# Performance work log

Measured on AMD Instinct MI355X. Metric: run time of the kernel, lower is better.

## Reference

```python
import jax, jax.numpy as jnp
import numpy as np

_R, _C = 64, 64
_N = _R * _C
_SEC_PER_A = 31556926.0
_K = 0.01        # sheet_conductivity
_ALPHA = 1.25    # sheet_flow_exp
_HR = 0.1        # bedrock_step_height
_LR = 2.0        # cavity_spacing
_A = 5e-25       # cavity_closure_coeff
_NEXP = 3        # Glen exponent


def _build_grid():
    idx = np.arange(_N).reshape(_R, _C)
    tail = np.concatenate([idx[:, :-1].ravel(), idx[:-1, :].ravel()]).astype(np.int32)
    head = np.concatenate([idx[:, 1:].ravel(), idx[1:, :].ravel()]).astype(np.int32)
    L = tail.size
    links_at_node = -np.ones((_N, 4), np.int32)
    adj = -np.ones((_N, 4), np.int32)
    cnt = np.zeros(_N, np.int32)
    for l in range(L):
        for a, b in ((tail[l], head[l]), (head[l], tail[l])):
            links_at_node[a, cnt[a]] = l
            adj[a, cnt[a]] = b
            cnt[a] += 1
    r, c = np.divmod(np.arange(_N), _C)
    status = ((r == 0) | (r == _R - 1) | (c == 0) | (c == _C - 1)).astype(np.int32)
    return tail, head, links_at_node, adj, status


def setup_inputs():
    key = jax.random.key(0)
    k = jax.random.split(key, 8)
    tail, head, links_at_node, adj, status = _build_grid()
    L = tail.size
    bedrock = jax.random.uniform(k[0], (_N,), jnp.float32, 0.0, 500.0)
    ice_thk = jax.random.uniform(k[1], (_N,), jnp.float32, 100.0, 1000.0)
    overburden = 917.0 * 9.81 * ice_thk
    base_potential = 1000.0 * 9.81 * bedrock + overburden
    potential = base_potential - 0.3 * overburden + 1e3 * jax.random.normal(k[2], (_N,), jnp.float32)
    sheet_thickness = jax.random.uniform(k[3], (_N,), jnp.float32, 0.01, 0.1)
    sliding_velocity = jax.random.uniform(k[4], (L,), jnp.float32, 10.0, 100.0)
    specific_melt_rate = jax.random.uniform(k[5], (_N,), jnp.float32, 1e-7, 1e-6)
    link_length = jnp.full((L,), 100.0, jnp.float32)
    adj_j = jnp.asarray(adj)
    # mean over ALL 4 slots, padded entries contribute 0 (matches original jnp.mean)
    adj_pot = jnp.mean(jnp.where(adj_j != -1, base_potential[adj_j], 0.0), axis=1)
    inflow = jnp.where(base_potential > adj_pot, 1, -1) * (jnp.asarray(status) > 0)
    return dict(
        base_potential=base_potential,
        overburden_pressure=overburden,
        specific_melt_rate=specific_melt_rate,
        sheet_thickness=sheet_thickness,
        potential=potential,
        sliding_velocity=sliding_velocity,
        link_length=link_length,
        link_tail=jnp.asarray(tail),
        link_head=jnp.asarray(head),
        links_at_node=jnp.asarray(links_at_node),
        inflow_outflow=inflow.astype(jnp.int32),
        dt=3600,
    )


def reference(base_potential, overburden_pressure, specific_melt_rate, sheet_thickness,
              potential, sliding_velocity, link_length, link_tail, link_head,
              links_at_node, inflow_outflow, dt):
    N = base_potential.shape[0]
    t, h = link_tail, link_head
    # --- elliptic operator assembly (per-link, scatter into dense [N,N]) ---
    sheets = 0.5 * (sheet_thickness[t] + sheet_thickness[h])
    inv_grad = jnp.abs((potential[t] - potential[h]) / link_length) ** (-0.5)
    c = -_K * sheets ** _ALPHA * link_length * inv_grad  # symmetric link coefficient (<0)
    dir_row = inflow_outflow == 1  # Dirichlet rows
    ct = jnp.where(dir_row[t], 0.0, c)  # contribution into row tail
    ch = jnp.where(dir_row[h], 0.0, c)  # contribution into row head
    M = (jnp.zeros((N, N), base_potential.dtype)
         .at[t, h].add(ct).at[h, t].add(ch)
         .at[t, t].add(-ct).at[h, h].add(-ch))
    M = jnp.where(dir_row[:, None], jnp.eye(N, dtype=M.dtype), M)
    forcing = jnp.where(dir_row, base_potential - overburden_pressure, specific_melt_rate)
    new_potential = jnp.linalg.solve(M, forcing)
    # --- sheet thickness: map_mean_of_links_to_node then Newton on node-local ODE ---
    valid = links_at_node != -1
    lv = (sliding_velocity / _SEC_PER_A)[links_at_node]  # [N,4]
    sliding = jnp.abs(jnp.sum(jnp.where(valid, lv, 0.0), axis=1)
                      / jnp.maximum(valid.sum(axis=1), 1))
    pressure = base_potential - new_potential
    dtf = jnp.asarray(dt, base_potential.dtype)
    # residual r(h) = h - h0 - dt*(sliding*(HR-h)/LR - A*P^n*h) is LINEAR in h,
    # so Newton converges in one exact step -> closed form:
    new_h = (sheet_thickness + dtf * sliding * _HR / _LR) / (
        1.0 + dtf * (sliding / _LR + _A * pressure ** _NEXP))
    return new_potential, new_h
```

## Files before the change

kernel.cpp:

```cpp
#include <hip/hip_runtime.h>
#include <math.h>


#define NT    512
#define NPT   8
#define NN    4096
#define NC    1024
#define NCC   256
#define CCIT  20
#define MAXIT 40

enum : int { RSHL1 = 0x101, RSHR1 = 0x111,
             ROR8 = 0x128, ROR12 = 0x12C, ROR14 = 0x12E, ROR15 = 0x12F,
             WSHL1 = 0x130, WSHR1 = 0x138 };

__device__ __forceinline__ void barL() {
    asm volatile("s_waitcnt lgkmcnt(0)" ::: "memory");
    __builtin_amdgcn_s_barrier();
    asm volatile("" ::: "memory");
}

template<int CTRL>
__device__ __forceinline__ float dppf(float x) {
    return __int_as_float(__builtin_amdgcn_update_dpp(
        __float_as_int(x), __float_as_int(x), CTRL, 0xF, 0xF, false));
}
template<int CTRL>
__device__ __forceinline__ double dppd(double x) {
    const int lo = __double2loint(x), hi = __double2hiint(x);
    const int l2 = __builtin_amdgcn_update_dpp(lo, lo, CTRL, 0xF, 0xF, false);
    const int h2 = __builtin_amdgcn_update_dpp(hi, hi, CTRL, 0xF, 0xF, false);
    return __hiloint2double(h2, l2);
}
__device__ __forceinline__ void pl16sw(int& a, int& b) {
    asm volatile("s_nop 1\n\tv_permlane16_swap_b32 %0, %1" : "+v"(a), "+v"(b));
}
__device__ __forceinline__ void pl32sw(int& a, int& b) {
    asm volatile("s_nop 1\n\tv_permlane32_swap_b32 %0, %1" : "+v"(a), "+v"(b));
}
__device__ __forceinline__ float shift_dn16(float x, bool inR2) {
    int a = __float_as_int(x), b = __float_as_int(x);
    pl16sw(a, b);
    int g = b, g2 = b;
    pl32sw(g, g2);
    return __int_as_float(inR2 ? g : a);
}
__device__ __forceinline__ float shift_up16(float x, bool inR1) {
    int a = __float_as_int(x), b = __float_as_int(x);
    pl16sw(a, b);
    int d1 = __float_as_int(x), d2 = __float_as_int(x);
    pl32sw(d1, d2);
    int e1 = d2, e2 = d2;
    pl16sw(e1, e2);
    return __int_as_float(inR1 ? e1 : b);
}
__device__ __forceinline__ double dsw32(double x) {
    int lo = __double2loint(x), hi = __double2hiint(x);
    int a = lo, b = lo; pl32sw(a, b);
    int c = hi, d = hi; pl32sw(c, d);
    return __hiloint2double(d, b);
}
__device__ __forceinline__ double dsw16(double x) {
    int lo = __double2loint(x), hi = __double2hiint(x);
    int a = lo, b = lo; pl16sw(a, b);
    int c = hi, d = hi; pl16sw(c, d);
    return __hiloint2double(d, b);
}

__global__ __launch_bounds__(NT, 1)
void sds_solver(const float* __restrict__ base_pot,
                const float* __restrict__ ovb,
                const float* __restrict__ melt,
                const float* __restrict__ sheet,
                const float* __restrict__ pot,
                const float* __restrict__ svel,
                const float* __restrict__ llen,
                const int*   __restrict__ ltail,
                const int*   __restrict__ lhead,
                const int*   __restrict__ lan,
                const int*   __restrict__ inflow,
                const int*   __restrict__ dt_raw,
                float* __restrict__ out,
                int N, int L)
{
    __shared__ __align__(16) float cW[NN], cE[NN], cN[NN], cS[NN];
    __shared__ __align__(16) float FD[NN];
    __shared__ __align__(16) float BNDA[8*128], BNDB[8*128];
    __shared__ __align__(16) float CB[32 + NC + 32];
    __shared__ __align__(16) float CB2[32 + NC + 32];
    __shared__ __align__(16) float EB[32 + NC + 32];
    __shared__ __align__(16) float IDC[32 + NC + 32];
    __shared__ __align__(16) float ccb[NCC];
    __shared__ __align__(16) float cWc_s[NC], cEc_s[NC], cNc_s[NC], cSc_s[NC], dc_s[NC];
    __shared__ double redp[32], redg[16];

    const int tid  = threadIdx.x;
    const int lane = tid & 63;
    const int wid  = tid >> 6;
    const int nb0  = (wid << 9) + lane;

    if (N != NN || L != 8064) return;

    const int dti = dt_raw[0];
    const float as_f = __int_as_float(dti);
    const double dtf = (as_f > 0.5f && as_f < 1.0e12f) ? (double)as_f : (double)dti;

    const float invthf = 0.8f;
    const float c1f = 0.2195122f, c2f = 0.9756098f;
    const float wA = 1.75f;

    {
        const float4 z4 = make_float4(0.f, 0.f, 0.f, 0.f);
        #pragma unroll
        for (int i = tid; i < NN/4; i += NT) {
            ((float4*)cW)[i] = z4; ((float4*)cE)[i] = z4;
            ((float4*)cN)[i] = z4; ((float4*)cS)[i] = z4;
        }
        if (tid < 32) {
            CB[tid]=0.f;  CB[32+NC+tid]=0.f;
            CB2[tid]=0.f; CB2[32+NC+tid]=0.f;
            EB[tid]=0.f;  EB[32+NC+tid]=0.f;
            IDC[tid]=0.f; IDC[32+NC+tid]=0.f;
        }
    }
    __syncthreads();

    for (int l = tid; l < 8064; l += NT) {
        int t, h;
        if (l < 4032) {
            const int r = l / 63;
            const int c2 = l - r * 63;
            t = (r << 6) + c2; h = t + 1;
        } else {
            t = l - 4032; h = t + 64;
        }
        const float sheets = 0.5f * (sheet[t] + sheet[h]);
        const float len = llen[l];
        const float grad = fabsf((pot[t] - pot[h]) / len);
        const float c = -0.01f * (sheets * sqrtf(sqrtf(sheets))) * len / sqrtf(grad);
        const bool dt_ = (inflow[t] == 1);
        const bool dh_ = (inflow[h] == 1);
        if (l < 4032) { cE[t] = dt_ ? 0.f : c; cW[h] = dh_ ? 0.f : c; }
        else          { cS[t] = dt_ ? 0.f : c; cN[h] = dh_ ? 0.f : c; }
    }
    __syncthreads();

    float cw[NPT], ce[NPT], cn[NPT], cs[NPT], dgf[NPT], invdf[NPT];
    double bb[NPT], gg[NPT], xv[NPT], rv[NPT];
    bool dirf[NPT];
    auto ldco = [&]() {
        #pragma unroll
        for (int k = 0; k < NPT; ++k) {
            const int n = nb0 + (k << 6);
            cw[k] = cW[n]; ce[k] = cE[n]; cn[k] = cN[n]; cs[k] = cS[n];
        }
    };
    ldco();
    double gsum = 0.0, gcnt = 0.0;
    #pragma unroll
    for (int k = 0; k < NPT; ++k) {
        const int n = nb0 + (k << 6);
        const bool dir = (inflow[n] == 1);
        const double g = (double)base_pot[n] - (double)ovb[n];
        const double d = -((double)cw[k] + (double)ce[k] + (double)cn[k] + (double)cs[k]);
        const double dg = (dir || d == 0.0) ? 1.0 : d;
        dgf[k] = (float)dg; invdf[k] = (float)(1.0 / dg);
        bb[k] = dir ? g : (double)melt[n];
        gg[k] = g; dirf[k] = dir;
        if (dir) { gsum += g; gcnt += 1.0; }
    }
    {
        #pragma unroll
        for (int off = 32; off > 0; off >>= 1) {
            gsum += __shfl_down(gsum, off, 64);
            gcnt += __shfl_down(gcnt, off, 64);
        }
        if (lane == 0) { redg[2*wid] = gsum; redg[2*wid+1] = gcnt; }
        __syncthreads();
        gsum = 0.0; gcnt = 0.0;
        #pragma unroll
        for (int w = 0; w < NT/64; ++w) { gsum += redg[2*w]; gcnt += redg[2*w+1]; }
    }
    const double gmean = gsum / (gcnt > 0.0 ? gcnt : 1.0);

    auto stB = [&](float* B, const float* v) {
        *(float2*)&B[(wid << 7) + (lane << 1)] = make_float2(v[0], v[7]);
    };
    float qf[NPT];
    auto spmvC = [&](const float* B, const float* vr) {
        const float nb = B[(((wid + 7) & 7) << 7) + (lane << 1) + 1];
        const float sb = B[(((wid + 1) & 7) << 7) + (lane << 1) + 0];
        #pragma unroll
        for (int k = 0; k < NPT; ++k) {
            const float wv = dppf<WSHR1>(vr[k]);
            const float ev = dppf<WSHL1>(vr[k]);
            const float nv = k ? vr[k-1] : nb;
            const float sv = (k < NPT-1) ? vr[k+1] : sb;
            qf[k] = dgf[k]*vr[k] + cw[k]*wv + ce[k]*ev + cn[k]*nv + cs[k]*sv;
        }
    };

    {
        float x0r[NPT];
        #pragma unroll
        for (int k = 0; k < NPT; ++k) {
            const float x0f = (float)(dirf[k] ? gg[k] : gmean);
            xv[k] = (double)x0f; x0r[k] = x0f;
        }
        stB(BNDA, x0r); __syncthreads();
        spmvC(BNDA, x0r);
        #pragma unroll
        for (int k = 0; k < NPT; ++k)
            rv[k] = dirf[k] ? 0.0 : (bb[k] - (double)qf[k]);
    }
    __syncthreads();

    {
        #pragma unroll
        for (int k = 0; k < NPT; ++k) {
            const int n = nb0 + (k << 6);
            if (lane != 0  && inflow[n-1]  == 1) cW[n] = 0.f;
            if (lane != 63 && inflow[n+1]  == 1) cE[n] = 0.f;
            if (n >= 64        && inflow[n-64] == 1) cN[n] = 0.f;
            if (n < NN-64      && inflow[n+64] == 1) cS[n] = 0.f;
            FD[n] = dirf[k] ? 0.f : dgf[k];
        }
    }
    __syncthreads();
    ldco();

    #pragma unroll
    for (int q = 0; q < 2; ++q) {
        const int I = 2*tid + q;
        const int R = tid >> 4, C = I & 31;
        const int na = 128*R + 2*C, nbq = na+1, nc_ = na+64, nd = na+65;
        cEc_s[I] = cE[nbq] + cE[nd];
        cWc_s[I] = cW[na] + cW[nc_];
        cNc_s[I] = cN[na] + cN[nbq];
        cSc_s[I] = cS[nc_] + cS[nd];
        const float d = FD[na]+FD[nbq]+FD[nc_]+FD[nd]
                      + 2.0f*(cE[na] + cE[nc_] + cS[na] + cS[nbq]);
        dc_s[I] = (d > 0.f) ? d : 1.0f;
    }
    __syncthreads();

    float cwc[2], cec[2], cnc[2], csc[2], dcr[2], invdc[2];
    {
        float2 t;
        t = *(float2*)&cWc_s[2*tid]; cwc[0]=t.x; cwc[1]=t.y;
        t = *(float2*)&cEc_s[2*tid]; cec[0]=t.x; cec[1]=t.y;
        t = *(float2*)&cNc_s[2*tid]; cnc[0]=t.x; cnc[1]=t.y;
        t = *(float2*)&cSc_s[2*tid]; csc[0]=t.x; csc[1]=t.y;
        t = *(float2*)&dc_s[2*tid];  dcr[0]=t.x; dcr[1]=t.y;
        invdc[0] = 1.0f/dcr[0]; invdc[1] = 1.0f/dcr[1];
        *(float2*)&IDC[32 + 2*tid] = make_float2(invdc[0], invdc[1]);
    }
    float cwcc[4], cecc[4], cncc[4], cscc[4], dccr[4], invdcc[4];
    if (tid < 64) {
        #pragma unroll
        for (int j = 0; j < 4; ++j) {
            const int Rc = ((tid >> 4) << 2) + j, Cc = tid & 15;
            const int IA = 64*Rc + 2*Cc, IB = IA+1, IC = IA+32, ID = IA+33;
            cecc[j] = cEc_s[IB] + cEc_s[ID];
            cwcc[j] = cWc_s[IA] + cWc_s[IC];
            cncc[j] = cNc_s[IA] + cNc_s[IB];
            cscc[j] = cSc_s[IC] + cSc_s[ID];
            const float d = dc_s[IA]+dc_s[IB]+dc_s[IC]+dc_s[ID]
                          + 2.0f*(cEc_s[IA] + cEc_s[IC] + cSc_s[IA] + cSc_s[IB]);
            dccr[j] = (d > 0.f) ? d : 1.0f;
            invdcc[j] = 1.0f/dccr[j];
        }
    }
    float c1cc[CCIT+1], c2cc[CCIT+1], invthcc;
    {
        const double a = 8e-3, b2 = 2.0;
        const double th = 0.5*(b2+a), de = 0.5*(b2-a), s1 = th/de;
        double rp = 1.0/s1;
        for (int j = 1; j <= CCIT; ++j) {
            const double rj = 1.0/(2.0*s1 - rp);
            c1cc[j] = (float)(rj*rp);
            c2cc[j] = (float)(2.0*rj/de);
            rp = rj;
        }
        invthcc = (float)(1.0/th);
    }
    auto cspmv = [&](const float* B_, float v0, float v1, float& q0, float& q1) {
        const float2 up = *(const float2*)&B_[2*tid];
        const float2 dn = *(const float2*)&B_[64 + 2*tid];
        const float wv = dppf<WSHR1>(v1);
        const float ev = dppf<WSHL1>(v0);
        q0 = dcr[0]*v0 + cwc[0]*wv + cec[0]*v1 + cnc[0]*up.x + csc[0]*dn.x;
        q1 = dcr[1]*v1 + cwc[1]*v0 + cec[1]*ev + cnc[1]*up.y + csc[1]*dn.y;
    };

    double rho_prev = 0.0, pap = 0.0, tol = 0.0;
    double pv[NPT], sv[NPT], rpv[NPT];
    #pragma unroll
    for (int k = 0; k < NPT; ++k) { pv[k]=0.0; sv[k]=0.0; rpv[k]=0.0; }

    for (int it = 0; it < MAXIT; ++it) {
        float f0[NPT], d0[NPT], d1[NPT], zpre[NPT];
        #pragma unroll
        for (int k = 0; k < NPT; ++k) { f0[k] = (float)rv[k] * invdf[k]; d0[k] = f0[k] * invthf; }
        stB(BNDA, d0); barL();
        spmvC(BNDA, d0);
        #pragma unroll
        for (int k = 0; k < NPT; ++k) {
            const float f1 = f0[k] - qf[k]*invdf[k];
            d1[k] = c1f*d0[k] + c2f*f1;
            zpre[k] = d0[k] + d1[k];
            f0[k] = f1;
        }
        stB(BNDB, d1); barL();
        spmvC(BNDB, d1);

        float r1[NPT], t2[NPT];
        #pragma unroll
        for (int k = 0; k < NPT; ++k) {
            const float fres = f0[k] - qf[k]*invdf[k];
            r1[k] = dirf[k] ? 0.f : dgf[k]*fres;
        }
        #pragma unroll
        for (int k = 0; k < NPT; ++k) t2[k] = r1[k] + dppf<WSHL1>(r1[k]);
        if ((lane & 1) == 0) {
            #pragma unroll
            for (int j = 0; j < 4; ++j)
                CB2[32 + ((wid << 2) + j)*32 + (lane >> 1)] = t2[2*j] + t2[2*j+1];
        }
        barL();

        float rc[2], f0c[2], d0c[2], d1c[2], qc0, qc1;
        {
            const float2 rcl = *(const float2*)&CB2[32 + 2*tid];
            rc[0] = rcl.x; rc[1] = rcl.y;
        }
        #pragma unroll
        for (int q = 0; q < 2; ++q) {
            f0c[q] = rc[q] * invdc[q];
            d0c[q] = f0c[q] * invthf;
        }
        {
            const float2 ru = *(const float2*)&CB2[2*tid];
            const float2 rd = *(const float2*)&CB2[64 + 2*tid];
            const float2 iu = *(const float2*)&IDC[2*tid];
            const float2 id = *(const float2*)&IDC[64 + 2*tid];
            const float wv = dppf<WSHR1>(d0c[1]);
            const float ev = dppf<WSHL1>(d0c[0]);
            qc0 = dcr[0]*d0c[0] + cwc[0]*wv + cec[0]*d0c[1]
                + cnc[0]*((ru.x*iu.x)*invthf) + csc[0]*((rd.x*id.x)*invthf);
            qc1 = dcr[1]*d0c[1] + cwc[1]*d0c[0] + cec[1]*ev
                + cnc[1]*((ru.y*iu.y)*invthf) + csc[1]*((rd.y*id.y)*invthf);
        }
        {
            const float f1a = f0c[0] - qc0*invdc[0];
            const float f1b = f0c[1] - qc1*invdc[1];
            d1c[0] = c1f*d0c[0] + c2f*f1a;
            d1c[1] = c1f*d0c[1] + c2f*f1b;
            f0c[0] = f1a; f0c[1] = f1b;
        }
        *(float2*)&EB[32 + 2*tid] = make_float2(d1c[0], d1c[1]);
        barL();
        cspmv(EB, d1c[0], d1c[1], qc0, qc1);
        {
            const float fra = f0c[0] - qc0*invdc[0];
            const float frb = f0c[1] - qc1*invdc[1];
            *(float2*)&CB[32 + 2*tid] = make_float2(dcr[0]*fra, dcr[1]*frb);
        }
        barL();

        if (tid < 64) {
            const int cc_c  = tid & 15;
            const int cc_rb = tid >> 4;
            const bool inR1 = (cc_rb == 1), inR2 = (cc_rb == 2);
            float fr[4], dr[4], zc[4];
            #pragma unroll
            for (int j = 0; j < 4; ++j) {
                const int IA = (((cc_rb << 2) + j) << 6) + (cc_c << 1);
                const float rcc = CB[32+IA] + CB[32+IA+1] + CB[32+IA+32] + CB[32+IA+33];
                fr[j] = rcc * invdcc[j];
                dr[j] = fr[j] * invthcc;
                zc[j] = dr[j];
            }
            for (int s = 1; s <= CCIT; ++s) {
                const float zN = shift_dn16(dr[3], inR2);
                const float zS = shift_up16(dr[0], inR1);
                float qcc[4];
                #pragma unroll
                for (int j = 0; j < 4; ++j) {
                    const float wj = dppf<RSHR1>(dr[j]);
                    const float ej = dppf<RSHL1>(dr[j]);
                    const float nj = j ? dr[j-1] : zN;
                    const float sj = (j < 3) ? dr[j+1] : zS;
                    qcc[j] = dccr[j]*dr[j] + cwcc[j]*wj + cecc[j]*ej
                           + cncc[j]*nj + cscc[j]*sj;
                }
                #pragma unroll
                for (int j = 0; j < 4; ++j) {
                    fr[j] -= qcc[j] * invdcc[j];
                    dr[j]  = c1cc[s]*dr[j] + c2cc[s]*fr[j];
                    zc[j] += dr[j];
                }
            }
            #pragma unroll
            for (int j = 0; j < 4; ++j)
                ccb[(((cc_rb << 2) + j) << 4) + cc_c] = zc[j];
        }
        barL();

        const float ecv = wA * ccb[16*(tid >> 5) + (tid & 15)];
        float zmc[2] = { d0c[0] + d1c[0] + ecv, d0c[1] + d1c[1] + ecv };
        {
            const float2 ru = *(const float2*)&CB2[2*tid];
            const float2 rd = *(const float2*)&CB2[64 + 2*tid];
            const float2 iu = *(const float2*)&IDC[2*tid];
            const float2 id = *(const float2*)&IDC[64 + 2*tid];
            const float2 du = *(const float2*)&EB[2*tid];
            const float2 dd = *(const float2*)&EB[64 + 2*tid];
            const int R = tid >> 4;
            const int Ru = (R > 0)  ? R - 1 : 0;
            const int Rd = (R < 31) ? R + 1 : 31;
            const float ecu = wA * ccb[(Ru >> 1)*16 + (tid & 15)];
            const float ecd = wA * ccb[(Rd >> 1)*16 + (tid & 15)];
            const float upx = ((ru.x*iu.x)*invthf + du.x) + ecu;
            const float upy = ((ru.y*iu.y)*invthf + du.y) + ecu;
            const float dnx = ((rd.x*id.x)*invthf + dd.x) + ecd;
            const float dny = ((rd.y*id.y)*invthf + dd.y) + ecd;
            const float wv = dppf<WSHR1>(zmc[1]);
            const float ev = dppf<WSHL1>(zmc[0]);
            qc0 = dcr[0]*zmc[0] + cwc[0]*wv + cec[0]*zmc[1] + cnc[0]*upx + csc[0]*dnx;
            qc1 = dcr[1]*zmc[1] + cwc[1]*zmc[0] + cec[1]*ev + cnc[1]*upy + csc[1]*dny;
        }
        float fmc[2] = { (rc[0]-qc0)*invdc[0], (rc[1]-qc1)*invdc[1] };
        float d0p[2] = { fmc[0]*invthf, fmc[1]*invthf };
        *(float2*)&CB[32 + 2*tid] = make_float2(d0p[0], d0p[1]);
        barL();
        cspmv(CB, d0p[0], d0p[1], qc0, qc1);
        {
            const float f1a = fmc[0] - qc0*invdc[0];
            const float f1b = fmc[1] - qc1*invdc[1];
            const float efa = zmc[0] + c1f*d0p[0] + c2f*f1a + d0p[0];
            const float efb = zmc[1] + c1f*d0p[1] + c2f*f1b + d0p[1];
            *(float2*)&EB[32 + 2*tid] = make_float2(efa, efb);
        }
        barL();

        float ec[4];
        #pragma unroll
        for (int j = 0; j < 4; ++j)
            ec[j] = EB[32 + ((wid << 2) + j)*32 + (lane >> 1)];
        float zmid[NPT], zf[NPT];
        #pragma unroll
        for (int k = 0; k < NPT; ++k)
            zmid[k] = zpre[k] + (dirf[k] ? 0.f : wA * ec[k >> 1]);
        stB(BNDA, zmid); barL();
        spmvC(BNDA, zmid);
        float fmid[NPT], d0q[NPT];
        #pragma unroll
        for (int k = 0; k < NPT; ++k) {
            fmid[k] = (float)rv[k]*invdf[k] - qf[k]*invdf[k];
            d0q[k]  = fmid[k] * invthf;
        }
        stB(BNDB, d0q); barL();
        spmvC(BNDB, d0q);
        #pragma unroll
        for (int k = 0; k < NPT; ++k) {
            const float f1 = fmid[k] - qf[k]*invdf[k];
            zf[k] = zmid[k] + d0q[k] + c1f*d0q[k] + c2f*f1;
        }
        stB(BNDA, zf); barL();
        spmvC(BNDA, zf);

        double rho_n = 0.0, rzp = 0.0, zw = 0.0, pw = 0.0;
        #pragma unroll
        for (int k = 0; k < NPT; ++k) {
            const double zk = (double)zf[k], wk = (double)qf[k];
            rho_n += rv[k]  * zk;
            rzp   += rpv[k] * zk;
            zw    += zk * wk;
            pw    += pv[k] * wk;
        }
        rho_n += dsw32(rho_n); rzp += dsw32(rzp); zw += dsw32(zw); pw += dsw32(pw);
        rho_n += dsw16(rho_n); rzp += dsw16(rzp); zw += dsw16(zw); pw += dsw16(pw);
        rho_n += dppd<ROR8 >(rho_n); rzp += dppd<ROR8 >(rzp); zw += dppd<ROR8 >(zw); pw += dppd<ROR8 >(pw);
        rho_n += dppd<ROR12>(rho_n); rzp += dppd<ROR12>(rzp); zw += dppd<ROR12>(zw); pw += dppd<ROR12>(pw);
        rho_n += dppd<ROR14>(rho_n); rzp += dppd<ROR14>(rzp); zw += dppd<ROR14>(zw); pw += dppd<ROR14>(pw);
        rho_n += dppd<ROR15>(rho_n); rzp += dppd<ROR15>(rzp); zw += dppd<ROR15>(zw); pw += dppd<ROR15>(pw);
        if (lane == 0) {
            redp[4*wid] = rho_n; redp[4*wid+1] = rzp;
            redp[4*wid+2] = zw;  redp[4*wid+3] = pw;
        }
        barL();
        rho_n = 0.0; rzp = 0.0; zw = 0.0; pw = 0.0;
        #pragma unroll
        for (int w = 0; w < NT/64; ++w) {
            rho_n += redp[4*w];   rzp += redp[4*w+1];
            zw    += redp[4*w+2]; pw  += redp[4*w+3];
        }

        if (it == 0) {
            tol = rho_n * 1e-3 + 1e-300;
            if (!(rho_n > 0.0)) break;
        } else if (rho_n <= tol || !(rho_n > 0.0)) break;
        const double beta = (it == 0) ? 0.0
                          : fmax(0.0, (rho_n - rzp) / rho_prev);
        pap = zw + beta * (2.0 * pw + beta * pap);
        if (!(pap > 0.0)) break;
        const double alpha = rho_n / pap;
        rho_prev = rho_n;
        #pragma unroll
        for (int k = 0; k < NPT; ++k) {
            rpv[k] = rv[k];
            pv[k] = (double)zf[k] + beta * pv[k];
            sv[k] = (double)qf[k] + beta * sv[k];
            xv[k] += alpha * pv[k];
            rv[k] -= alpha * sv[k];
        }
    }

    #pragma unroll
    for (int k = 0; k < NPT; ++k) {
        const int n = nb0 + (k << 6);
        const int r = (wid << 3) + k, c2 = lane;
        const double x = dirf[k] ? gg[k] : xv[k];

        const int hb = r * 63 + c2;
        float sva = 0.0f; int cnt = 0;
        if (c2 > 0)  { sva += svel[hb - 1];       cnt++; }
        if (c2 < 63) { sva += svel[hb];           cnt++; }
        if (r  > 0)  { sva += svel[4032 + n - 64]; cnt++; }
        if (r  < 63) { sva += svel[4032 + n];      cnt++; }
        const double sliding =
            fabs((double)sva / 31556926.0 / (double)(cnt > 0 ? cnt : 1));
        const double P   = (double)base_pot[n] - x;
        const double num = (double)sheet[n] + dtf * sliding * 0.1 / 2.0;
        const double den = 1.0 + dtf * (sliding / 2.0 + 5e-25 * P * P * P);
        out[n]      = (float)x;
        out[NN + n] = (float)(num / den);
    }
}

extern "C" void kernel_launch(void* const* d_in, const int* in_sizes, int n_in,
                              void* d_out, int out_size, void* d_ws, size_t ws_size,
                              hipStream_t stream) {
    const float* base_pot = (const float*)d_in[0];
    const float* ovb      = (const float*)d_in[1];
    const float* melt     = (const float*)d_in[2];
    const float* sheet    = (const float*)d_in[3];
    const float* pot      = (const float*)d_in[4];
    const float* svel     = (const float*)d_in[5];
    const float* llen     = (const float*)d_in[6];
    const int*   ltail    = (const int*)d_in[7];
    const int*   lhead    = (const int*)d_in[8];
    const int*   lan      = (const int*)d_in[9];
    const int*   inflow   = (const int*)d_in[10];
    const int*   dt_raw   = (const int*)d_in[11];
    float* out = (float*)d_out;
    const int N = in_sizes[0];
    const int L = in_sizes[5];

    hipLaunchKernelGGL(sds_solver, dim3(1), dim3(NT), 0, stream,
                       base_pot, ovb, melt, sheet, pot, svel, llen,
                       ltail, lhead, lan, inflow, dt_raw, out, N, L);
}
```

Baseline: 133.6 us.

## Double block to 1024 threads with four rows per thread

Raises the single workgroup from 512 to 1024 threads (16 waves), so each thread owns 4 grid rows instead of 8. The coarse-grid step now maps one coarse cell per thread instead of two, so the per-thread loops and float2 accesses become scalar ones. The goal is to shorten the serial per-thread work in every PCG iteration of this single-block solver. In exchange, each block-wide reduction now combines 16 wave partials instead of 8, barriers span more waves, and the per-thread register budget is halved at 1024 threads.

Measured after the change: 178.8 us. 33.8% more time.

```diff
diff --git a/kernel.cpp b/kernel.cpp
--- a/kernel.cpp
+++ b/kernel.cpp
@@ -2,8 +2,9 @@
 #include <math.h>
 
 
-#define NT    512
-#define NPT   8
+#define NT    1024
+#define NPT   4
+#define NW    16
 #define NN    4096
 #define NC    1024
 #define NCC   256
@@ -85,19 +86,19 @@
 {
     __shared__ __align__(16) float cW[NN], cE[NN], cN[NN], cS[NN];
     __shared__ __align__(16) float FD[NN];
-    __shared__ __align__(16) float BNDA[8*128], BNDB[8*128];
+    __shared__ __align__(16) float BNDA[NW*128], BNDB[NW*128];
     __shared__ __align__(16) float CB[32 + NC + 32];
     __shared__ __align__(16) float CB2[32 + NC + 32];
     __shared__ __align__(16) float EB[32 + NC + 32];
     __shared__ __align__(16) float IDC[32 + NC + 32];
     __shared__ __align__(16) float ccb[NCC];
     __shared__ __align__(16) float cWc_s[NC], cEc_s[NC], cNc_s[NC], cSc_s[NC], dc_s[NC];
-    __shared__ double redp[32], redg[16];
+    __shared__ double redp[4*NW], redg[2*NW];
 
     const int tid  = threadIdx.x;
     const int lane = tid & 63;
     const int wid  = tid >> 6;
-    const int nb0  = (wid << 9) + lane;
+    const int nb0  = (wid << 8) + lane;
 
     if (N != NN || L != 8064) return;
 
@@ -179,17 +180,17 @@
         __syncthreads();
         gsum = 0.0; gcnt = 0.0;
         #pragma unroll
-        for (int w = 0; w < NT/64; ++w) { gsum += redg[2*w]; gcnt += redg[2*w+1]; }
+        for (int w = 0; w < NW; ++w) { gsum += redg[2*w]; gcnt += redg[2*w+1]; }
     }
     const double gmean = gsum / (gcnt > 0.0 ? gcnt : 1.0);
 
     auto stB = [&](float* B, const float* v) {
-        *(float2*)&B[(wid << 7) + (lane << 1)] = make_float2(v[0], v[7]);
+        *(float2*)&B[(wid << 7) + (lane << 1)] = make_float2(v[0], v[NPT-1]);
     };
     float qf[NPT];
     auto spmvC = [&](const float* B, const float* vr) {
-        const float nb = B[(((wid + 7) & 7) << 7) + (lane << 1) + 1];
-        const float sb = B[(((wid + 1) & 7) << 7) + (lane << 1) + 0];
+        const float nb = B[(((wid + NW-1) & (NW-1)) << 7) + (lane << 1) + 1];
+        const float sb = B[(((wid + 1) & (NW-1)) << 7) + (lane << 1) + 0];
         #pragma unroll
         for (int k = 0; k < NPT; ++k) {
             const float wv = dppf<WSHR1>(vr[k]);
@@ -229,31 +230,25 @@
     __syncthreads();
     ldco();
 
-    #pragma unroll
-    for (int q = 0; q < 2; ++q) {
-        const int I = 2*tid + q;
-        const int R = tid >> 4, C = I & 31;
+    {
+        const int R = tid >> 5, C = tid & 31;
         const int na = 128*R + 2*C, nbq = na+1, nc_ = na+64, nd = na+65;
-        cEc_s[I] = cE[nbq] + cE[nd];
-        cWc_s[I] = cW[na] + cW[nc_];
-        cNc_s[I] = cN[na] + cN[nbq];
-        cSc_s[I] = cS[nc_] + cS[nd];
+        cEc_s[tid] = cE[nbq] + cE[nd];
+        cWc_s[tid] = cW[na] + cW[nc_];
+        cNc_s[tid] = cN[na] + cN[nbq];
+        cSc_s[tid] = cS[nc_] + cS[nd];
         const float d = FD[na]+FD[nbq]+FD[nc_]+FD[nd]
                       + 2.0f*(cE[na] + cE[nc_] + cS[na] + cS[nbq]);
-        dc_s[I] = (d > 0.f) ? d : 1.0f;
+        dc_s[tid] = (d > 0.f) ? d : 1.0f;
     }
     __syncthreads();
 
-    float cwc[2], cec[2], cnc[2], csc[2], dcr[2], invdc[2];
-    {
-        float2 t;
-        t = *(float2*)&cWc_s[2*tid]; cwc[0]=t.x; cwc[1]=t.y;
-        t = *(float2*)&cEc_s[2*tid]; cec[0]=t.x; cec[1]=t.y;
-        t = *(float2*)&cNc_s[2*tid]; cnc[0]=t.x; cnc[1]=t.y;
-        t = *(float2*)&cSc_s[2*tid]; csc[0]=t.x; csc[1]=t.y;
-        t = *(float2*)&dc_s[2*tid];  dcr[0]=t.x; dcr[1]=t.y;
-        invdc[0] = 1.0f/dcr[0]; invdc[1] = 1.0f/dcr[1];
-        *(float2*)&IDC[32 + 2*tid] = make_float2(invdc[0], invdc[1]);
+    float cwc, cec, cnc, csc, dcr, invdc;
+    {
+        cwc = cWc_s[tid]; cec = cEc_s[tid];
+        cnc = cNc_s[tid]; csc = cSc_s[tid];
+        dcr = dc_s[tid];  invdc = 1.0f/dcr;
+        IDC[32 + tid] = invdc;
     }
     float cwcc[4], cecc[4], cncc[4], cscc[4], dccr[4], invdcc[4];
     if (tid < 64) {
@@ -284,13 +279,12 @@
         }
         invthcc = (float)(1.0/th);
     }
-    auto cspmv = [&](const float* B_, float v0, float v1, float& q0, float& q1) {
-        const float2 up = *(const float2*)&B_[2*tid];
-        const float2 dn = *(const float2*)&B_[64 + 2*tid];
-        const float wv = dppf<WSHR1>(v1);
-        const float ev = dppf<WSHL1>(v0);
-        q0 = dcr[0]*v0 + cwc[0]*wv + cec[0]*v1 + cnc[0]*up.x + csc[0]*dn.x;
-        q1 = dcr[1]*v1 + cwc[1]*v0 + cec[1]*ev + cnc[1]*up.y + csc[1]*dn.y;
+    auto cspmv = [&](const float* B_, float v, float& q) {
+        const float up = B_[tid];
+        const float dn = B_[64 + tid];
+        const float wv = dppf<WSHR1>(v);
+        const float ev = dppf<WSHL1>(v);
+        q = dcr*v + cwc*wv + cec*ev + cnc*up + csc*dn;
     };
 
     double rho_prev = 0.0, pap = 0.0, tol = 0.0;
@@ -324,47 +318,34 @@
         for (int k = 0; k < NPT; ++k) t2[k] = r1[k] + dppf<WSHL1>(r1[k]);
         if ((lane & 1) == 0) {
             #pragma unroll
-            for (int j = 0; j < 4; ++j)
-                CB2[32 + ((wid << 2) + j)*32 + (lane >> 1)] = t2[2*j] + t2[2*j+1];
-        }
-        barL();
-
-        float rc[2], f0c[2], d0c[2], d1c[2], qc0, qc1;
+            for (int j = 0; j < 2; ++j)
+                CB2[32 + ((wid << 1) + j)*32 + (lane >> 1)] = t2[2*j] + t2[2*j+1];
+        }
+        barL();
+
+        float rc, f0c, d0c, d1c, qc;
+        rc = CB2[32 + tid];
+        f0c = rc * invdc;
+        d0c = f0c * invthf;
         {
-            const float2 rcl = *(const float2*)&CB2[32 + 2*tid];
-            rc[0] = rcl.x; rc[1] = rcl.y;
-        }
-        #pragma unroll
-        for (int q = 0; q < 2; ++q) {
-            f0c[q] = rc[q] * invdc[q];
-            d0c[q] = f0c[q] * invthf;
+            const float ru = CB2[tid],      rd = CB2[64 + tid];
+            const float iu = IDC[tid],      id = IDC[64 + tid];
+            const float wv = dppf<WSHR1>(d0c);
+            const float ev = dppf<WSHL1>(d0c);
+            qc = dcr*d0c + cwc*wv + cec*ev
+               + cnc*((ru*iu)*invthf) + csc*((rd*id)*invthf);
         }
         {
-            const float2 ru = *(const float2*)&CB2[2*tid];
-            const float2 rd = *(const float2*)&CB2[64 + 2*tid];
-            const float2 iu = *(const float2*)&IDC[2*tid];
-            const float2 id = *(const float2*)&IDC[64 + 2*tid];
-            const float wv = dppf<WSHR1>(d0c[1]);
-            const float ev = dppf<WSHL1>(d0c[0]);
-            qc0 = dcr[0]*d0c[0] + cwc[0]*wv + cec[0]*d0c[1]
-                + cnc[0]*((ru.x*iu.x)*invthf) + csc[0]*((rd.x*id.x)*invthf);
-            qc1 = dcr[1]*d0c[1] + cwc[1]*d0c[0] + cec[1]*ev
-                + cnc[1]*((ru.y*iu.y)*invthf) + csc[1]*((rd.y*id.y)*invthf);
-        }
+            const float f1 = f0c - qc*invdc;
+            d1c = c1f*d0c + c2f*f1;
+            f0c = f1;
+        }
+        EB[32 + tid] = d1c;
+        barL();
+        cspmv(EB, d1c, qc);
         {
-            const float f1a = f0c[0] - qc0*invdc[0];
-            const float f1b = f0c[1] - qc1*invdc[1];
-            d1c[0] = c1f*d0c[0] + c2f*f1a;
-            d1c[1] = c1f*d0c[1] + c2f*f1b;
-            f0c[0] = f1a; f0c[1] = f1b;
-        }
-        *(float2*)&EB[32 + 2*tid] = make_float2(d1c[0], d1c[1]);
-        barL();
-        cspmv(EB, d1c[0], d1c[1], qc0, qc1);
-        {
-            const float fra = f0c[0] - qc0*invdc[0];
-            const float frb = f0c[1] - qc1*invdc[1];
-            *(float2*)&CB[32 + 2*tid] = make_float2(dcr[0]*fra, dcr[1]*frb);
+            const float fra = f0c - qc*invdc;
+            CB[32 + tid] = dcr*fra;
         }
         barL();
 
@@ -407,47 +388,38 @@
         }
         barL();
 
-        const float ecv = wA * ccb[16*(tid >> 5) + (tid & 15)];
-        float zmc[2] = { d0c[0] + d1c[0] + ecv, d0c[1] + d1c[1] + ecv };
+        const int Rq = tid >> 5, Cq = tid & 31;
+        const float ecv = wA * ccb[(Rq >> 1)*16 + (Cq >> 1)];
+        float zmc = d0c + d1c + ecv;
         {
-            const float2 ru = *(const float2*)&CB2[2*tid];
-            const float2 rd = *(const float2*)&CB2[64 + 2*tid];
-            const float2 iu = *(const float2*)&IDC[2*tid];
-            const float2 id = *(const float2*)&IDC[64 + 2*tid];
-            const float2 du = *(const float2*)&EB[2*tid];
-            const float2 dd = *(const float2*)&EB[64 + 2*tid];
-            const int R = tid >> 4;
-            const int Ru = (R > 0)  ? R - 1 : 0;
-            const int Rd = (R < 31) ? R + 1 : 31;
-            const float ecu = wA * ccb[(Ru >> 1)*16 + (tid & 15)];
-            const float ecd = wA * ccb[(Rd >> 1)*16 + (tid & 15)];
-            const float upx = ((ru.x*iu.x)*invthf + du.x) + ecu;
-            const float upy = ((ru.y*iu.y)*invthf + du.y) + ecu;
-            const float dnx = ((rd.x*id.x)*invthf + dd.x) + ecd;
-            const float dny = ((rd.y*id.y)*invthf + dd.y) + ecd;
-            const float wv = dppf<WSHR1>(zmc[1]);
-            const float ev = dppf<WSHL1>(zmc[0]);
-            qc0 = dcr[0]*zmc[0] + cwc[0]*wv + cec[0]*zmc[1] + cnc[0]*upx + csc[0]*dnx;
-            qc1 = dcr[1]*zmc[1] + cwc[1]*zmc[0] + cec[1]*ev + cnc[1]*upy + csc[1]*dny;
-        }
-        float fmc[2] = { (rc[0]-qc0)*invdc[0], (rc[1]-qc1)*invdc[1] };
-        float d0p[2] = { fmc[0]*invthf, fmc[1]*invthf };
-        *(float2*)&CB[32 + 2*tid] = make_float2(d0p[0], d0p[1]);
-        barL();
-        cspmv(CB, d0p[0], d0p[1], qc0, qc1);
+            const float ru = CB2[tid],      rd = CB2[64 + tid];
+            const float iu = IDC[tid],      id = IDC[64 + tid];
+            const float du = EB[tid],       dd = EB[64 + tid];
+            const int Ru = (Rq > 0)  ? Rq - 1 : 0;
+            const int Rd = (Rq < 31) ? Rq + 1 : 31;
+            const float ecu = wA * ccb[(Ru >> 1)*16 + (Cq >> 1)];
+            const float ecd = wA * ccb[(Rd >> 1)*16 + (Cq >> 1)];
+            const float upv = ((ru*iu)*invthf + du) + ecu;
+            const float dnv = ((rd*id)*invthf + dd) + ecd;
+            const float wv = dppf<WSHR1>(zmc);
+            const float ev = dppf<WSHL1>(zmc);
+            qc = dcr*zmc + cwc*wv + cec*ev + cnc*upv + csc*dnv;
+        }
+        float fmc = (rc - qc)*invdc;
+        float d0p = fmc*invthf;
+        CB[32 + tid] = d0p;
+        barL();
+        cspmv(CB, d0p, qc);
         {
-            const float f1a = fmc[0] - qc0*invdc[0];
-            const float f1b = fmc[1] - qc1*invdc[1];
-            const float efa = zmc[0] + c1f*d0p[0] + c2f*f1a + d0p[0];
-            const float efb = zmc[1] + c1f*d0p[1] + c2f*f1b + d0p[1];
-            *(float2*)&EB[32 + 2*tid] = make_float2(efa, efb);
-        }
-        barL();
-
-        float ec[4];
-        #pragma unroll
-        for (int j = 0; j < 4; ++j)
-            ec[j] = EB[32 + ((wid << 2) + j)*32 + (lane >> 1)];
+            const float f1 = fmc - qc*invdc;
+            EB[32 + tid] = zmc + c1f*d0p + c2f*f1 + d0p;
+        }
+        barL();
+
+        float ec[2];
+        #pragma unroll
+        for (int j = 0; j < 2; ++j)
+            ec[j] = EB[32 + ((wid << 1) + j)*32 + (lane >> 1)];
         float zmid[NPT], zf[NPT];
         #pragma unroll
         for (int k = 0; k < NPT; ++k)
@@ -492,7 +464,7 @@
         barL();
         rho_n = 0.0; rzp = 0.0; zw = 0.0; pw = 0.0;
         #pragma unroll
-        for (int w = 0; w < NT/64; ++w) {
+        for (int w = 0; w < NW; ++w) {
             rho_n += redp[4*w];   rzp += redp[4*w+1];
             zw    += redp[4*w+2]; pw  += redp[4*w+3];
         }
@@ -520,7 +492,7 @@
     #pragma unroll
     for (int k = 0; k < NPT; ++k) {
         const int n = nb0 + (k << 6);
-        const int r = (wid << 3) + k, c2 = lane;
+        const int r = (wid << 2) + k, c2 = lane;
         const double x = dirf[k] ? gg[k] : xv[k];
 
         const int hb = r * 63 + c2;
```
